# Kernel tuning notes

Measured on AMD Instinct MI355X. Metric: run time of the kernel, lower is better.

Reference implementation:

```python
import jax, jax.numpy as jnp
import numpy as np

B, T, D, N, K, H, F = 2, 2048, 2048, 8, 1, 256, 16384
BIG_NEG = -2.3819763e+38


def _apply_rope(x, positions, max_wavelength=10000):
    # x: [B, L, heads, H], positions: [B, L] int32
    half = x.shape[-1] // 2
    freq_exponents = (2.0 / x.shape[-1]) * jnp.arange(half, dtype=jnp.float32)
    timescale = max_wavelength ** freq_exponents  # [half]
    radians = positions[..., None] / timescale[None, None, :]  # [B, L, half] fp32
    radians = radians[..., None, :]  # [B, L, 1, half]
    sin, cos = jnp.sin(radians), jnp.cos(radians)
    x1, x2 = jnp.split(x, 2, axis=-1)
    res = jnp.concatenate([x1 * cos - x2 * sin, x2 * cos + x1 * sin], axis=-1)
    return res.astype(x.dtype)


def _rmsnorm(x, scale):
    var = jnp.mean(jnp.square(x.astype(jnp.float32)), axis=-1, keepdims=True)
    normed = x * jax.lax.rsqrt(var + 1e-6)
    return (normed * (1 + scale)).astype(x.dtype)


def setup_inputs() -> dict:
    key = jax.random.key(0)
    ks = jax.random.split(key, 6)
    x = jax.random.normal(ks[0], (B, T, D), dtype=jnp.float32)
    positions = jnp.broadcast_to(jnp.arange(T, dtype=jnp.int32), (B, T))
    # causal mask, asserted shape (B, 1, T, S)
    attn_mask = jnp.broadcast_to(jnp.tril(jnp.ones((T, T), dtype=bool))[None, None], (B, 1, T, T))
    q_w = jax.random.normal(ks[1], (N, D, H), dtype=jnp.float32) * (1.0 / np.sqrt(D))
    kv_w = jax.random.normal(ks[2], (2, K, D, H), dtype=jnp.float32) * (1.0 / np.sqrt(D))
    attn_vec_w = jax.random.normal(ks[3], (N, H, D), dtype=jnp.float32) * (1.0 / np.sqrt(N * H))
    gating_w = jax.random.normal(ks[4], (2, D, F), dtype=jnp.float32) * (1.0 / np.sqrt(D))
    linear_w = jax.random.normal(ks[5], (F, D), dtype=jnp.float32) * (1.0 / np.sqrt(F))
    pre_attn_scale = jnp.zeros((D,), dtype=jnp.float32)
    pre_ffw_scale = jnp.zeros((D,), dtype=jnp.float32)
    return {"x": x, "positions": positions, "attn_mask": attn_mask, "q_w": q_w,
            "kv_w": kv_w, "attn_vec_w": attn_vec_w, "gating_w": gating_w,
            "linear_w": linear_w, "pre_attn_scale": pre_attn_scale,
            "pre_ffw_scale": pre_ffw_scale}


def reference(x, positions, attn_mask, q_w, kv_w, attn_vec_w, gating_w, linear_w,
              pre_attn_scale, pre_ffw_scale):
    dtype = x.dtype
    # --- pre-attention RMSNorm ---
    h = _rmsnorm(x, pre_attn_scale)
    # --- GQA projections (num_kv_heads != num_heads branch) ---
    q = jnp.einsum('btd,ndh->btnh', h, q_w)            # [B, T, N, H]
    kv = jnp.einsum('bsd,ckdh->cbskh', h, kv_w)        # [2, B, T, K, H]
    k, v = kv[0], kv[1]
    q = _apply_rope(q, positions) * (H ** -0.5)
    k = _apply_rope(k, positions)
    # --- grouped attention ---
    qg = q.reshape(q.shape[0], q.shape[1], K, N // K, H)  # B T K G H
    logits = jnp.einsum('btkgh,bskh->bkgts', qg, k, preferred_element_type=jnp.float32)
    masked = jnp.where(attn_mask[:, :, None, :, :], logits, BIG_NEG)
    probs = jax.nn.softmax(masked, axis=-1).astype(dtype)
    enc = jnp.einsum('bkgts,bskh->btkgh', probs, v)
    enc = enc.reshape(enc.shape[0], enc.shape[1], N, H)   # B T (K G) H
    attn_out = jnp.einsum('btnh,nhd->btd', enc, attn_vec_w)
    x = x + attn_out
    # --- GeGLU MLP ---
    h2 = _rmsnorm(x, pre_ffw_scale)
    gate = jax.nn.gelu(jnp.dot(h2, gating_w[0]))  # flax nn.gelu default: approximate
    acts = gate * jnp.dot(h2, gating_w[1])
    x = x + jnp.dot(acts, linear_w)
    return x
```

## Files before the change

### kernel.cpp

```cpp
#include <hip/hip_runtime.h>
#include <hip/hip_bf16.h>
#include <math.h>


using bf16 = __hip_bfloat16;
typedef short bf16x8 __attribute__((ext_vector_type(8)));
typedef float f32x4 __attribute__((ext_vector_type(4)));

__device__ __forceinline__ void gld_lds16(const bf16* g, bf16* l) {
    __builtin_amdgcn_global_load_lds(
        (const __attribute__((address_space(1))) void*)g,
        (__attribute__((address_space(3))) void*)l, 16, 0, 0);
}

__global__ __launch_bounds__(256, 2)
void gemm_bt(const bf16* __restrict__ A, const bf16* __restrict__ Bm,
             void* __restrict__ Cv, const float* __restrict__ res,
             int K, int lda, int ldb, int ldc,
             long sAb, long sAn, long sBb, long sBn, long sCb, long sCn,
             int nInner, int epi)
{
    __shared__ bf16 As[128 * 32];
    __shared__ bf16 Bs[128 * 32];

    const int zb = blockIdx.z / nInner;
    const int zn = blockIdx.z - zb * nInner;
    A  += (long)zb * sAb + (long)zn * sAn;
    Bm += (long)zb * sBb + (long)zn * sBn;
    const long coff = (long)zb * sCb + (long)zn * sCn;

    const int tid  = threadIdx.x;
    const int lane = tid & 63;
    const int wave = tid >> 6;
    const int wm = wave >> 1;
    const int wn = wave & 1;
    const int lr = lane & 15;
    const int lq = lane >> 4;

    const long m_blk = (long)blockIdx.y * 128;
    const long n_blk = (long)blockIdx.x * 128;

    f32x4 acc[4][4] = {};

    const int c0 = wave * 64 + lane;
    const int c1 = c0 + 256;
    const int am0 = c0 >> 2, am1 = c1 >> 2;
    const int ak0 = ((c0 & 3) ^ ((am0 >> 1) & 3)) * 8;
    const int ak1 = ((c1 & 3) ^ ((am1 >> 1) & 3)) * 8;
    const long aoff0 = (m_blk + am0) * (long)lda + ak0;
    const long aoff1 = (m_blk + am1) * (long)lda + ak1;
    const long boff0 = (n_blk + am0) * (long)ldb + ak0;
    const long boff1 = (n_blk + am1) * (long)ldb + ak1;
    bf16* lA0 = &As[(wave * 64) * 8];
    bf16* lA1 = &As[(256 + wave * 64) * 8];
    bf16* lB0 = &Bs[(wave * 64) * 8];
    bf16* lB1 = &Bs[(256 + wave * 64) * 8];

    for (int k0 = 0; k0 < K; k0 += 32) {
        gld_lds16(A + aoff0 + k0, lA0);
        gld_lds16(A + aoff1 + k0, lA1);
        gld_lds16(Bm + boff0 + k0, lB0);
        gld_lds16(Bm + boff1 + k0, lB1);
        __syncthreads();

        bf16x8 af[4], bfr[4];
        #pragma unroll
        for (int t = 0; t < 4; ++t) {
            const int mr = wm * 64 + t * 16 + lr;
            af[t]  = *(const bf16x8*)&As[(mr * 4 + (lq ^ ((mr >> 1) & 3))) * 8];
            const int nr = wn * 64 + t * 16 + lr;
            bfr[t] = *(const bf16x8*)&Bs[(nr * 4 + (lq ^ ((nr >> 1) & 3))) * 8];
        }
        #pragma unroll
        for (int mt = 0; mt < 4; ++mt)
            #pragma unroll
            for (int nt = 0; nt < 4; ++nt)
                acc[mt][nt] = __builtin_amdgcn_mfma_f32_16x16x32_bf16(
                    af[mt], bfr[nt], acc[mt][nt], 0, 0, 0);
        __syncthreads();
    }

    #pragma unroll
    for (int mt = 0; mt < 4; ++mt) {
        #pragma unroll
        for (int nt = 0; nt < 4; ++nt) {
            const long col = n_blk + wn * 64 + nt * 16 + lr;
            #pragma unroll
            for (int r = 0; r < 4; ++r) {
                const long row = m_blk + wm * 64 + mt * 16 + lq * 4 + r;
                const long idx = coff + row * (long)ldc + col;
                const float v = acc[mt][nt][r];
                if (epi == 0)      ((bf16*)Cv)[idx]  = __float2bfloat16(v);
                else if (epi == 1) ((float*)Cv)[idx] = v;
                else               ((float*)Cv)[idx] = v + res[row * (long)ldc + col];
            }
        }
    }
}

__global__ __launch_bounds__(256)
void transpose_f2b(const float* __restrict__ in, bf16* __restrict__ out,
                   int ldin, int ldout, long inB, long outB)
{
    __shared__ float tile[32][33];
    in  += (long)blockIdx.z * inB;
    out += (long)blockIdx.z * outB;
    const int r0 = blockIdx.y * 32, c0 = blockIdx.x * 32;
    const int tx = threadIdx.x & 31, ty = threadIdx.x >> 5;
    #pragma unroll
    for (int i = 0; i < 32; i += 8)
        tile[ty + i][tx] = in[(long)(r0 + ty + i) * ldin + c0 + tx];
    __syncthreads();
    #pragma unroll
    for (int i = 0; i < 32; i += 8)
        out[(long)(c0 + ty + i) * ldout + r0 + tx] = __float2bfloat16(tile[tx][ty + i]);
}

__global__ __launch_bounds__(256)
void transpose_b2b(const bf16* __restrict__ in, bf16* __restrict__ out,
                   int ldin, int ldout, long inB, long outB)
{
    __shared__ bf16 tile[32][33];
    in  += (long)blockIdx.z * inB;
    out += (long)blockIdx.z * outB;
    const int r0 = blockIdx.y * 32, c0 = blockIdx.x * 32;
    const int tx = threadIdx.x & 31, ty = threadIdx.x >> 5;
    #pragma unroll
    for (int i = 0; i < 32; i += 8)
        tile[ty + i][tx] = in[(long)(r0 + ty + i) * ldin + c0 + tx];
    __syncthreads();
    #pragma unroll
    for (int i = 0; i < 32; i += 8)
        out[(long)(c0 + ty + i) * ldout + r0 + tx] = tile[tx][ty + i];
}

__global__ __launch_bounds__(256)
void rmsnorm_k(const float* __restrict__ x, const float* __restrict__ scale,
               bf16* __restrict__ out)
{
    const long row = blockIdx.x;
    const float* xr = x + row * 2048;
    const int tid = threadIdx.x;
    const float4 a = ((const float4*)xr)[tid];
    const float4 b = ((const float4*)xr)[tid + 256];
    float ss = a.x*a.x + a.y*a.y + a.z*a.z + a.w*a.w
             + b.x*b.x + b.y*b.y + b.z*b.z + b.w*b.w;
    for (int o = 32; o; o >>= 1) ss += __shfl_down(ss, o, 64);
    __shared__ float red[4];
    const int lane = tid & 63, wave = tid >> 6;
    if (lane == 0) red[wave] = ss;
    __syncthreads();
    const float inv = rsqrtf((red[0] + red[1] + red[2] + red[3]) * (1.f / 2048.f) + 1e-6f);
    const float4 s0 = ((const float4*)scale)[tid];
    const float4 s1 = ((const float4*)scale)[tid + 256];
    bf16* orow = out + row * 2048;
    const int i0 = tid * 4, i1 = 1024 + tid * 4;
    orow[i0 + 0] = __float2bfloat16(a.x * inv * (1.f + s0.x));
    orow[i0 + 1] = __float2bfloat16(a.y * inv * (1.f + s0.y));
    orow[i0 + 2] = __float2bfloat16(a.z * inv * (1.f + s0.z));
    orow[i0 + 3] = __float2bfloat16(a.w * inv * (1.f + s0.w));
    orow[i1 + 0] = __float2bfloat16(b.x * inv * (1.f + s1.x));
    orow[i1 + 1] = __float2bfloat16(b.y * inv * (1.f + s1.y));
    orow[i1 + 2] = __float2bfloat16(b.z * inv * (1.f + s1.z));
    orow[i1 + 3] = __float2bfloat16(b.w * inv * (1.f + s1.w));
}

__global__ __launch_bounds__(256)
void rope_k(bf16* __restrict__ qkv, const int* __restrict__ positions)
{
    const long row = blockIdx.x;
    const float pos = (float)positions[row];
    bf16* rp = qkv + row * 2560;
    for (int w = threadIdx.x; w < 1152; w += 256) {
        const int head = w >> 7;
        const int j = w & 127;
        const int base = head * 256;
        const float x1 = __bfloat162float(rp[base + j]);
        const float x2 = __bfloat162float(rp[base + 128 + j]);
        const float ts = powf(10000.f, (float)j * (1.f / 128.f));
        const float rad = pos / ts;
        const float s = sinf(rad), c = cosf(rad);
        const float sc = (head < 8) ? 0.0625f : 1.0f;
        rp[base + j]       = __float2bfloat16((x1 * c - x2 * s) * sc);
        rp[base + 128 + j] = __float2bfloat16((x2 * c + x1 * s) * sc);
    }
}

__global__ __launch_bounds__(256)
void softmax_causal(const float* __restrict__ logits, bf16* __restrict__ probs)
{
    const int t = blockIdx.x;
    const long rowid = (long)blockIdx.y * 2048 + t;
    const float* lrow = logits + rowid * 2048;
    bf16* prow = probs + rowid * 2048;
    const int tid = threadIdx.x;
    const float4 a = ((const float4*)lrow)[tid];
    const float4 b = ((const float4*)lrow)[tid + 256];
    const int s0 = tid * 4, s1 = 1024 + tid * 4;
    float va[8] = {a.x, a.y, a.z, a.w, b.x, b.y, b.z, b.w};
    int   sidx[8] = {s0, s0+1, s0+2, s0+3, s1, s1+1, s1+2, s1+3};

    float mx = -3.0e38f;
    #pragma unroll
    for (int i = 0; i < 8; ++i) if (sidx[i] <= t) mx = fmaxf(mx, va[i]);
    for (int o = 32; o; o >>= 1) mx = fmaxf(mx, __shfl_down(mx, o, 64));
    __shared__ float red[4];
    const int lane = tid & 63, wave = tid >> 6;
    if (lane == 0) red[wave] = mx;
    __syncthreads();
    mx = fmaxf(fmaxf(red[0], red[1]), fmaxf(red[2], red[3]));
    __syncthreads();

    float e[8]; float sum = 0.f;
    #pragma unroll
    for (int i = 0; i < 8; ++i) {
        e[i] = (sidx[i] <= t) ? __expf(va[i] - mx) : 0.f;
        sum += e[i];
    }
    for (int o = 32; o; o >>= 1) sum += __shfl_down(sum, o, 64);
    if (lane == 0) red[wave] = sum;
    __syncthreads();
    sum = red[0] + red[1] + red[2] + red[3];
    const float inv = 1.f / sum;
    #pragma unroll
    for (int i = 0; i < 8; ++i) prow[sidx[i]] = __float2bfloat16(e[i] * inv);
}

__global__ __launch_bounds__(256)
void gelu_mul_k(const bf16* __restrict__ g, bf16* __restrict__ acts)
{
    const long v = (long)blockIdx.x * 256 + threadIdx.x;
    const long f4 = v * 4;
    const long t = f4 >> 14;
    const int  f = (int)(f4 & 16383);
    const bf16* g0 = g + t * 32768 + f;
    const bf16* g1 = g0 + 16384;
    bf16* o = acts + t * 16384 + f;
    #pragma unroll
    for (int i = 0; i < 4; ++i) {
        const float xg = __bfloat162float(g0[i]);
        const float xv = __bfloat162float(g1[i]);
        const float c = xg + 0.044715f * xg * xg * xg;
        const float ge = 0.5f * xg * (1.f + tanhf(0.7978845608f * c));
        o[i] = __float2bfloat16(ge * xv);
    }
}

static inline void launch_gemm(const bf16* A, const bf16* Bm, void* C,
                               const float* res, int M, int N, int K,
                               int lda, int ldb, int ldc,
                               long sAb, long sAn, long sBb, long sBn,
                               long sCb, long sCn, int nOuter, int nInner,
                               int epi, hipStream_t s)
{
    dim3 g(N / 128, M / 128, nOuter * nInner);
    gemm_bt<<<g, dim3(256), 0, s>>>(A, Bm, C, res, K, lda, ldb, ldc,
                                    sAb, sAn, sBb, sBn, sCb, sCn, nInner, epi);
}

extern "C" void kernel_launch(void* const* d_in, const int* in_sizes, int n_in,
                              void* d_out, int out_size, void* d_ws, size_t ws_size,
                              hipStream_t stream)
{
    const float* x          = (const float*)d_in[0];
    const int*   positions  = (const int*)d_in[1];
    const float* q_w        = (const float*)d_in[3];
    const float* kv_w       = (const float*)d_in[4];
    const float* attn_vec_w = (const float*)d_in[5];
    const float* gating_w   = (const float*)d_in[6];
    const float* linear_w   = (const float*)d_in[7];
    const float* pre_attn_s = (const float*)d_in[8];
    const float* pre_ffw_s  = (const float*)d_in[9];
    float* out = (float*)d_out;

    char* p = (char*)d_ws;
    auto alloc = [&](size_t bytes) { char* r = p; p += (bytes + 255) & ~(size_t)255; return r; };
    bf16*  Wqkv   = (bf16*)alloc(2560UL * 2048 * 2);
    bf16*  Wo     = (bf16*)alloc(2048UL * 2048 * 2);
    bf16*  Wg     = (bf16*)alloc(32768UL * 2048 * 2);
    bf16*  Wl     = (bf16*)alloc(2048UL * 16384 * 2);
    bf16*  h      = (bf16*)alloc(4096UL * 2048 * 2);
    bf16*  qkv    = (bf16*)alloc(4096UL * 2560 * 2);
    bf16*  vt     = (bf16*)alloc(2UL * 256 * 2048 * 2);
    float* xmid   = (float*)alloc(4096UL * 2048 * 4);
    bf16*  enc    = (bf16*)alloc(4096UL * 2048 * 2);
    float* logits = (float*)alloc(16UL * 2048 * 2048 * 4);
    bf16*  probs  = (bf16*)alloc(16UL * 2048 * 2048 * 2);
    bf16*  gbuf   = (bf16*)logits;
    bf16*  acts   = probs;
    if ((size_t)(p - (char*)d_ws) > ws_size) return;

    transpose_f2b<<<dim3(8, 64, 8), 256, 0, stream>>>(q_w, Wqkv, 256, 2048,
                                                      2048L * 256, 256L * 2048);
    transpose_f2b<<<dim3(8, 64, 2), 256, 0, stream>>>(kv_w, Wqkv + 2048L * 2048,
                                                      256, 2048, 2048L * 256, 256L * 2048);
    transpose_f2b<<<dim3(64, 64, 1), 256, 0, stream>>>(attn_vec_w, Wo, 2048, 2048, 0, 0);
    transpose_f2b<<<dim3(512, 64, 2), 256, 0, stream>>>(gating_w, Wg, 16384, 2048,
                                                        2048L * 16384, 16384L * 2048);
    transpose_f2b<<<dim3(64, 512, 1), 256, 0, stream>>>(linear_w, Wl, 2048, 16384, 0, 0);

    rmsnorm_k<<<4096, 256, 0, stream>>>(x, pre_attn_s, h);
    launch_gemm(h, Wqkv, qkv, nullptr, 4096, 2560, 2048, 2048, 2048, 2560,
                0, 0, 0, 0, 0, 0, 1, 1, 0, stream);
    rope_k<<<4096, 256, 0, stream>>>(qkv, positions);
    transpose_b2b<<<dim3(8, 64, 2), 256, 0, stream>>>(qkv + 2304, vt, 2560, 2048,
                                                      2048L * 2560, 256L * 2048);
    launch_gemm(qkv, qkv + 2048, logits, nullptr, 2048, 2048, 256, 2560, 2560, 2048,
                2048L * 2560, 256, 2048L * 2560, 0,
                8L * 2048 * 2048, 2048L * 2048, 2, 8, 1, stream);
    softmax_causal<<<dim3(2048, 16), 256, 0, stream>>>(logits, probs);
    launch_gemm(probs, vt, enc, nullptr, 2048, 256, 2048, 2048, 2048, 2048,
                8L * 2048 * 2048, 2048L * 2048, 256L * 2048, 0,
                2048L * 2048, 256, 2, 8, 0, stream);
    launch_gemm(enc, Wo, xmid, x, 4096, 2048, 2048, 2048, 2048, 2048,
                0, 0, 0, 0, 0, 0, 1, 1, 2, stream);

    rmsnorm_k<<<4096, 256, 0, stream>>>(xmid, pre_ffw_s, h);
    launch_gemm(h, Wg, gbuf, nullptr, 4096, 32768, 2048, 2048, 2048, 32768,
                0, 0, 0, 0, 0, 0, 1, 1, 0, stream);
    gelu_mul_k<<<65536, 256, 0, stream>>>(gbuf, acts);
    launch_gemm(acts, Wl, out, xmid, 4096, 2048, 16384, 16384, 16384, 2048,
                0, 0, 0, 0, 0, 0, 1, 1, 2, stream);
}
```

Baseline: 2.268 ms.

## Fuse GeGLU into gating GEMM, bf16 logits, grouped tile rasterization

Interleaves the two gating weight matrices row by row so each GEMM tile holds matching gate and value columns. A new epilogue pairs them with a lane shuffle, applies a sigmoid-form tanh-approximate GELU and writes the activations directly, which removes the separate gelu kernel and the round trip through a 4096x32768 intermediate. Logits are now stored and read as bf16 instead of fp32, halving softmax traffic at some precision cost. GEMM blocks are also remapped with grouped (GROUP=8) rasterization to improve L2 reuse.

```diff
diff --git a/kernel.cpp b/kernel.cpp
--- a/kernel.cpp
+++ b/kernel.cpp
@@ -28,6 +28,17 @@
     A  += (long)zb * sAb + (long)zn * sAn;
     Bm += (long)zb * sBb + (long)zn * sBn;
     const long coff = (long)zb * sCb + (long)zn * sCn;
+
+    const int GROUP = 8;
+    const int num_n = gridDim.x, num_m = gridDim.y;
+    const int pid = blockIdx.y * num_n + blockIdx.x;
+    const int band = GROUP * num_n;
+    const int group_id = pid / band;
+    const int first_m = group_id * GROUP;
+    const int gsz = min(num_m - first_m, GROUP);
+    const int in_group = pid - group_id * band;
+    const int pid_m = first_m + (in_group % gsz);
+    const int pid_n = in_group / gsz;
 
     const int tid  = threadIdx.x;
     const int lane = tid & 63;
@@ -37,8 +48,8 @@
     const int lr = lane & 15;
     const int lq = lane >> 4;
 
-    const long m_blk = (long)blockIdx.y * 128;
-    const long n_blk = (long)blockIdx.x * 128;
+    const long m_blk = (long)pid_m * 128;
+    const long n_blk = (long)pid_n * 128;
 
     f32x4 acc[4][4] = {};
 
@@ -88,11 +99,24 @@
             #pragma unroll
             for (int r = 0; r < 4; ++r) {
                 const long row = m_blk + wm * 64 + mt * 16 + lq * 4 + r;
-                const long idx = coff + row * (long)ldc + col;
                 const float v = acc[mt][nt][r];
-                if (epi == 0)      ((bf16*)Cv)[idx]  = __float2bfloat16(v);
-                else if (epi == 1) ((float*)Cv)[idx] = v;
-                else               ((float*)Cv)[idx] = v + res[row * (long)ldc + col];
+                if (epi == 0) {
+                    ((bf16*)Cv)[coff + row * (long)ldc + col] = __float2bfloat16(v);
+                } else if (epi == 1) {
+                    ((float*)Cv)[coff + row * (long)ldc + col] = v;
+                } else if (epi == 2) {
+                    ((float*)Cv)[coff + row * (long)ldc + col] =
+                        v + res[row * (long)ldc + col];
+                } else {
+                    const float pv = __shfl_xor(v, 1, 64);
+                    const float g0 = (lr & 1) ? pv : v;
+                    const float g1 = (lr & 1) ? v : pv;
+                    const float u = g0 + 0.044715f * g0 * g0 * g0;
+                    const float act = g0 / (1.f + __expf(-1.5957691216f * u)) * g1;
+                    if (!(lr & 1))
+                        ((bf16*)Cv)[row * (long)ldc + (col >> 1)] =
+                            __float2bfloat16(act);
+                }
             }
         }
     }
@@ -100,7 +124,7 @@
 
 __global__ __launch_bounds__(256)
 void transpose_f2b(const float* __restrict__ in, bf16* __restrict__ out,
-                   int ldin, int ldout, long inB, long outB)
+                   int ldin, int ldout, long inB, long outB, int rowMul)
 {
     __shared__ float tile[32][33];
     in  += (long)blockIdx.z * inB;
@@ -113,7 +137,8 @@
     __syncthreads();
     #pragma unroll
     for (int i = 0; i < 32; i += 8)
-        out[(long)(c0 + ty + i) * ldout + r0 + tx] = __float2bfloat16(tile[tx][ty + i]);
+        out[(long)(c0 + ty + i) * rowMul * ldout + r0 + tx] =
+            __float2bfloat16(tile[tx][ty + i]);
 }
 
 __global__ __launch_bounds__(256)
@@ -187,22 +212,23 @@
 }
 
 __global__ __launch_bounds__(256)
-void softmax_causal(const float* __restrict__ logits, bf16* __restrict__ probs)
+void softmax_causal(const bf16* __restrict__ logits, bf16* __restrict__ probs)
 {
     const int t = blockIdx.x;
     const long rowid = (long)blockIdx.y * 2048 + t;
-    const float* lrow = logits + rowid * 2048;
+    const bf16* lrow = logits + rowid * 2048;
     bf16* prow = probs + rowid * 2048;
     const int tid = threadIdx.x;
-    const float4 a = ((const float4*)lrow)[tid];
-    const float4 b = ((const float4*)lrow)[tid + 256];
-    const int s0 = tid * 4, s1 = 1024 + tid * 4;
-    float va[8] = {a.x, a.y, a.z, a.w, b.x, b.y, b.z, b.w};
-    int   sidx[8] = {s0, s0+1, s0+2, s0+3, s1, s1+1, s1+2, s1+3};
+    const bf16x8 raw = *(const bf16x8*)(lrow + tid * 8);
+    float va[8];
+    #pragma unroll
+    for (int i = 0; i < 8; ++i)
+        va[i] = __uint_as_float(((unsigned)(unsigned short)raw[i]) << 16);
+    const int s0 = tid * 8;
 
     float mx = -3.0e38f;
     #pragma unroll
-    for (int i = 0; i < 8; ++i) if (sidx[i] <= t) mx = fmaxf(mx, va[i]);
+    for (int i = 0; i < 8; ++i) if (s0 + i <= t) mx = fmaxf(mx, va[i]);
     for (int o = 32; o; o >>= 1) mx = fmaxf(mx, __shfl_down(mx, o, 64));
     __shared__ float red[4];
     const int lane = tid & 63, wave = tid >> 6;
@@ -214,7 +240,7 @@
     float e[8]; float sum = 0.f;
     #pragma unroll
     for (int i = 0; i < 8; ++i) {
-        e[i] = (sidx[i] <= t) ? __expf(va[i] - mx) : 0.f;
+        e[i] = (s0 + i <= t) ? __expf(va[i] - mx) : 0.f;
         sum += e[i];
     }
     for (int o = 32; o; o >>= 1) sum += __shfl_down(sum, o, 64);
@@ -223,27 +249,7 @@
     sum = red[0] + red[1] + red[2] + red[3];
     const float inv = 1.f / sum;
     #pragma unroll
-    for (int i = 0; i < 8; ++i) prow[sidx[i]] = __float2bfloat16(e[i] * inv);
-}
-
-__global__ __launch_bounds__(256)
-void gelu_mul_k(const bf16* __restrict__ g, bf16* __restrict__ acts)
-{
-    const long v = (long)blockIdx.x * 256 + threadIdx.x;
-    const long f4 = v * 4;
-    const long t = f4 >> 14;
-    const int  f = (int)(f4 & 16383);
-    const bf16* g0 = g + t * 32768 + f;
-    const bf16* g1 = g0 + 16384;
-    bf16* o = acts + t * 16384 + f;
-    #pragma unroll
-    for (int i = 0; i < 4; ++i) {
-        const float xg = __bfloat162float(g0[i]);
-        const float xv = __bfloat162float(g1[i]);
-        const float c = xg + 0.044715f * xg * xg * xg;
-        const float ge = 0.5f * xg * (1.f + tanhf(0.7978845608f * c));
-        o[i] = __float2bfloat16(ge * xv);
-    }
+    for (int i = 0; i < 8; ++i) prow[s0 + i] = __float2bfloat16(e[i] * inv);
 }
 
 static inline void launch_gemm(const bf16* A, const bf16* Bm, void* C,
@@ -284,20 +290,19 @@
     bf16*  vt     = (bf16*)alloc(2UL * 256 * 2048 * 2);
     float* xmid   = (float*)alloc(4096UL * 2048 * 4);
     bf16*  enc    = (bf16*)alloc(4096UL * 2048 * 2);
-    float* logits = (float*)alloc(16UL * 2048 * 2048 * 4);
+    bf16*  logits = (bf16*)alloc(16UL * 2048 * 2048 * 2);
     bf16*  probs  = (bf16*)alloc(16UL * 2048 * 2048 * 2);
-    bf16*  gbuf   = (bf16*)logits;
-    bf16*  acts   = probs;
+    bf16*  acts   = logits;
     if ((size_t)(p - (char*)d_ws) > ws_size) return;
 
     transpose_f2b<<<dim3(8, 64, 8), 256, 0, stream>>>(q_w, Wqkv, 256, 2048,
-                                                      2048L * 256, 256L * 2048);
+                                                      2048L * 256, 256L * 2048, 1);
     transpose_f2b<<<dim3(8, 64, 2), 256, 0, stream>>>(kv_w, Wqkv + 2048L * 2048,
-                                                      256, 2048, 2048L * 256, 256L * 2048);
-    transpose_f2b<<<dim3(64, 64, 1), 256, 0, stream>>>(attn_vec_w, Wo, 2048, 2048, 0, 0);
+                                                      256, 2048, 2048L * 256, 256L * 2048, 1);
+    transpose_f2b<<<dim3(64, 64, 1), 256, 0, stream>>>(attn_vec_w, Wo, 2048, 2048, 0, 0, 1);
     transpose_f2b<<<dim3(512, 64, 2), 256, 0, stream>>>(gating_w, Wg, 16384, 2048,
-                                                        2048L * 16384, 16384L * 2048);
-    transpose_f2b<<<dim3(64, 512, 1), 256, 0, stream>>>(linear_w, Wl, 2048, 16384, 0, 0);
+                                                        2048L * 16384, 2048, 2);
+    transpose_f2b<<<dim3(64, 512, 1), 256, 0, stream>>>(linear_w, Wl, 2048, 16384, 0, 0, 1);
 
     rmsnorm_k<<<4096, 256, 0, stream>>>(x, pre_attn_s, h);
     launch_gemm(h, Wqkv, qkv, nullptr, 4096, 2560, 2048, 2048, 2048, 2560,
@@ -307,7 +312,7 @@
                                                       2048L * 2560, 256L * 2048);
     launch_gemm(qkv, qkv + 2048, logits, nullptr, 2048, 2048, 256, 2560, 2560, 2048,
                 2048L * 2560, 256, 2048L * 2560, 0,
-                8L * 2048 * 2048, 2048L * 2048, 2, 8, 1, stream);
+                8L * 2048 * 2048, 2048L * 2048, 2, 8, 0, stream);
     softmax_causal<<<dim3(2048, 16), 256, 0, stream>>>(logits, probs);
     launch_gemm(probs, vt, enc, nullptr, 2048, 256, 2048, 2048, 2048, 2048,
                 8L * 2048 * 2048, 2048L * 2048, 256L * 2048, 0,
@@ -316,9 +321,8 @@
                 0, 0, 0, 0, 0, 0, 1, 1, 2, stream);
 
     rmsnorm_k<<<4096, 256, 0, stream>>>(xmid, pre_ffw_s, h);
-    launch_gemm(h, Wg, gbuf, nullptr, 4096, 32768, 2048, 2048, 2048, 32768,
-                0, 0, 0, 0, 0, 0, 1, 1, 0, stream);
-    gelu_mul_k<<<65536, 256, 0, stream>>>(gbuf, acts);
+    launch_gemm(h, Wg, acts, nullptr, 4096, 32768, 2048, 2048, 2048, 16384,
+                0, 0, 0, 0, 0, 0, 1, 1, 3, stream);
     launch_gemm(acts, Wl, out, xmid, 4096, 2048, 16384, 16384, 16384, 2048,
                 0, 0, 0, 0, 0, 0, 1, 1, 2, stream);
 }
```

Measured after the change: 2.113 ms. -6.9%, faster.
